# Optimization experiments

Hardware: AMD Instinct MI355X
Metric: run time of the kernel (lower is better)

The kernel has to match this reference:

```python
import jax, jax.numpy as jnp
import numpy as np

NUM_GROUPS = 32
NUM_HEADS = 8
EPS = 1e-5


def setup_inputs() -> dict:
    key = jax.random.key(0)
    ks = jax.random.split(key, 4)
    b, c, h, w = 16, 512, 32, 32
    x = jax.random.normal(ks[0], (b, c, h, w), dtype=jnp.float32)
    norm_w = jnp.ones((c,), dtype=jnp.float32)
    norm_b = jnp.zeros((c,), dtype=jnp.float32)
    qkv_w = jax.random.normal(ks[1], (3 * c, c), dtype=jnp.float32) * (1.0 / np.sqrt(c))
    qkv_b = jnp.zeros((3 * c,), dtype=jnp.float32)
    proj_w = jax.random.normal(ks[2], (c, c), dtype=jnp.float32) * (1.0 / np.sqrt(c))
    proj_b = jnp.zeros((c,), dtype=jnp.float32)
    return {"x": x, "norm_w": norm_w, "norm_b": norm_b,
            "qkv_w": qkv_w, "qkv_b": qkv_b, "proj_w": proj_w, "proj_b": proj_b}


def group_norm(x, weight, bias):
    b, c, h, w = x.shape
    xg = x.reshape(b, NUM_GROUPS, c // NUM_GROUPS, h * w)
    mean = xg.mean(axis=(2, 3), keepdims=True)
    var = xg.var(axis=(2, 3), keepdims=True)
    xn = (xg - mean) * jax.lax.rsqrt(var + EPS)
    xn = xn.reshape(b, c, h, w)
    return xn * weight[None, :, None, None] + bias[None, :, None, None]


def reference(x, norm_w, norm_b, qkv_w, qkv_b, proj_w, proj_b):
    b, c, h, w = x.shape
    n = h * w
    head = NUM_HEADS
    ch = c // head

    x_norm = group_norm(x, norm_w, norm_b)
    # 1x1 conv == channel matmul: [b,3c,n]
    xf = x_norm.reshape(b, c, n)
    qkv = jnp.einsum('oc,bcn->bon', qkv_w, xf) + qkv_b[None, :, None]
    q, k, v = jnp.split(qkv, 3, axis=1)  # each [b,c,n]
    q = q.reshape(b, head, ch, n) * (ch ** -0.5)
    k = k.reshape(b, head, ch, n)
    v = v.reshape(b, head, ch, n)

    attn = jnp.einsum('bhcn,bhcm->bhnm', q, k)
    attn = jax.nn.softmax(attn, axis=-1)
    out = jnp.einsum('bhnm,bhcm->bhcn', attn, v)  # [b,head,ch,n]
    out = out.reshape(b, c, n)
    out = jnp.einsum('oc,bcn->bon', proj_w, out) + proj_b[None, :, None]
    return x + out.reshape(b, c, h, w)
```

## Files before the change

### kernel.cpp

```cpp
#include <hip/hip_runtime.h>

typedef short short8 __attribute__((ext_vector_type(8)));
typedef short short4v __attribute__((ext_vector_type(4)));
typedef float f32x4 __attribute__((ext_vector_type(4)));

#define B_   16
#define C_   512
#define N_   1024
#define NH_  8
#define CH_  64
#define G_   32
#define CPG_ 16

__device__ inline float b2f(unsigned int u) {
    union { unsigned int i; float f; } v; v.i = u << 16; return v.f;
}
__device__ inline unsigned short f2b(float f) {
    union { float f; unsigned int i; } v; v.f = f;
    unsigned int r = v.i + 0x7fffu + ((v.i >> 16) & 1u);
    return (unsigned short)(r >> 16);
}
__device__ inline unsigned int pack2(float a, float b) {
    return (unsigned int)f2b(a) | ((unsigned int)f2b(b) << 16);
}
__device__ inline unsigned int asu(float f) {
    union { float f; unsigned int i; } v; v.f = f; return v.i;
}
__device__ inline unsigned int packtr(float a, float b) {
    return __builtin_amdgcn_perm(asu(b), asu(a), 0x07060302u);
}
__device__ inline void gload16(const void* g, void* l) {
    __builtin_amdgcn_global_load_lds(
        (const __attribute__((address_space(1))) void*)g,
        (__attribute__((address_space(3))) void*)l, 16, 0, 0);
}

__global__ __launch_bounds__(256) void gnconv_kernel(const float* __restrict__ x,
                                                     const float* __restrict__ nw,
                                                     const float* __restrict__ nb,
                                                     unsigned short* __restrict__ xnT,
                                                     const float* __restrict__ qkvw,
                                                     const float* __restrict__ projw,
                                                     unsigned short* __restrict__ wq,
                                                     unsigned short* __restrict__ wp)
{
    __shared__ float red[8];
    int t = threadIdx.x;

    if (blockIdx.x >= 512) {
        const int NQ = 3 * C_ * C_;
        int idx = (((int)blockIdx.x - 512) * 256 + t) * 8;
        const float* src; unsigned short* dst; int j;
        if (idx < NQ) { src = qkvw;  dst = wq; j = idx; }
        else          { src = projw; dst = wp; j = idx - NQ; }
        float4 u0 = *(const float4*)(src + j);
        float4 u1 = *(const float4*)(src + j + 4);
        uint4 p;
        p.x = pack2(u0.x, u0.y); p.y = pack2(u0.z, u0.w);
        p.z = pack2(u1.x, u1.y); p.w = pack2(u1.z, u1.w);
        *(uint4*)(dst + j) = p;
        return;
    }

    int b = blockIdx.x >> 5, g = blockIdx.x & 31;
    const float* base = x + ((size_t)(b * C_ + g * CPG_)) * N_;

    float s = 0.f, ss = 0.f;
    for (int it = 0; it < 16; ++it) {
        int idx = (it * 256 + t) * 4;
        float4 u = *(const float4*)(base + idx);
        s  += u.x + u.y + u.z + u.w;
        ss += u.x * u.x + u.y * u.y + u.z * u.z + u.w * u.w;
    }
#pragma unroll
    for (int off = 1; off < 64; off <<= 1) {
        s  += __shfl_xor(s, off);
        ss += __shfl_xor(ss, off);
    }
    int wv = t >> 6;
    if ((t & 63) == 0) { red[wv * 2] = s; red[wv * 2 + 1] = ss; }
    __syncthreads();
    s  = red[0] + red[2] + red[4] + red[6];
    ss = red[1] + red[3] + red[5] + red[7];
    float mean = s * (1.f / 16384.f);
    float var  = ss * (1.f / 16384.f) - mean * mean;
    float rstd = rsqrtf(var + 1e-5f);

    float sc[16], sh[16];
#pragma unroll
    for (int ch = 0; ch < 16; ++ch) {
        float wv_ = nw[g * CPG_ + ch];
        float bv_ = nb[g * CPG_ + ch];
        sc[ch] = wv_ * rstd;
        sh[ch] = bv_ - mean * sc[ch];
    }

#pragma unroll
    for (int nbi = 0; nbi < 2; ++nbi) {
        int n = nbi * 512 + t * 2;
        float2 v[16];
#pragma unroll
        for (int ch = 0; ch < 16; ++ch)
            v[ch] = *(const float2*)(base + (size_t)ch * N_ + n);
#pragma unroll
        for (int col = 0; col < 2; ++col) {
            float f[16];
#pragma unroll
            for (int ch = 0; ch < 16; ++ch) {
                float xv = col ? v[ch].y : v[ch].x;
                f[ch] = xv * sc[ch] + sh[ch];
            }
            uint4 o0, o1;
            o0.x = pack2(f[0], f[1]);  o0.y = pack2(f[2], f[3]);
            o0.z = pack2(f[4], f[5]);  o0.w = pack2(f[6], f[7]);
            o1.x = pack2(f[8], f[9]);  o1.y = pack2(f[10], f[11]);
            o1.z = pack2(f[12], f[13]); o1.w = pack2(f[14], f[15]);
            unsigned short* dst = xnT + ((size_t)(b * N_ + n + col)) * C_ + g * CPG_;
            *(uint4*)dst = o0;
            *(uint4*)(dst + 8) = o1;
        }
    }
}

__global__ __launch_bounds__(256) void qkv_kernel(const unsigned short* __restrict__ w,
                                                  const float* __restrict__ bias,
                                                  const unsigned short* __restrict__ xnT,
                                                  unsigned short* __restrict__ qT,
                                                  unsigned short* __restrict__ kT,
                                                  unsigned short* __restrict__ vv)
{
    __shared__ unsigned short Als[128 * 64], Bls[128 * 64];
    int t = threadIdx.x;
    int n0 = blockIdx.x * 128, m0 = blockIdx.y * 128, b = blockIdx.z;
    int lane = t & 63, wv = t >> 6;
    int l = lane & 15, qd = lane >> 4;
    int wm = (wv >> 1) * 64, wn = (wv & 1) * 64;
    f32x4 acc[4][4] = {};
    const unsigned short* Bbase = xnT + ((size_t)(b * N_ + n0)) * C_;

    int grow = lane >> 3, gcol = ((lane & 7) ^ grow) * 8;
    const unsigned short* pA[4]; const unsigned short* pB[4];
    unsigned short* lA[4]; unsigned short* lB[4];
#pragma unroll
    for (int g = 0; g < 4; ++g) {
        int r = wv * 32 + g * 8 + grow;
        pA[g] = w + (size_t)(m0 + r) * C_ + gcol;
        pB[g] = Bbase + (size_t)r * C_ + gcol;
        lA[g] = &Als[(wv * 32 + g * 8) * 64];
        lB[g] = &Bls[(wv * 32 + g * 8) * 64];
    }

    for (int kk = 0; kk < 8; ++kk) {
        int ko = kk * 64;
#pragma unroll
        for (int g = 0; g < 4; ++g) {
            gload16(pA[g] + ko, lA[g]);
            gload16(pB[g] + ko, lB[g]);
        }
        __builtin_amdgcn_s_waitcnt(0);
        __syncthreads();
#pragma unroll
        for (int ks = 0; ks < 2; ++ks) {
            short8 aF[4], bF[4];
#pragma unroll
            for (int i = 0; i < 4; ++i) {
                int ra = wm + i * 16 + l;
                aF[i] = *(const short8*)&Als[ra * 64 + (((ks * 4 + qd) ^ (l & 7)) * 8)];
                int rb = wn + i * 16 + l;
                bF[i] = *(const short8*)&Bls[rb * 64 + (((ks * 4 + qd) ^ (l & 7)) * 8)];
            }
#pragma unroll
            for (int mt = 0; mt < 4; ++mt)
#pragma unroll
                for (int nt = 0; nt < 4; ++nt)
                    acc[mt][nt] = __builtin_amdgcn_mfma_f32_16x16x32_bf16(aF[mt], bF[nt], acc[mt][nt], 0, 0, 0);
        }
        __syncthreads();
    }

    int o_base = m0 + wm;
    int sec = o_base >> 9;
    int oc = o_base & 511;
    int h = oc >> 6;
    float bv[4][4];
#pragma unroll
    for (int mt = 0; mt < 4; ++mt)
#pragma unroll
        for (int r = 0; r < 4; ++r)
            bv[mt][r] = bias[o_base + mt * 16 + qd * 4 + r];

    if (sec < 2) {
        unsigned short* dst = (sec == 0) ? qT : kT;
        float scl = (sec == 0) ? (0.125f * 1.44269504f) : 1.0f;
#pragma unroll
        for (int mt = 0; mt < 4; ++mt)
#pragma unroll
            for (int nt = 0; nt < 4; ++nt) {
                int n = n0 + wn + nt * 16 + l;
                ushort4 o;
                o.x = f2b((acc[mt][nt][0] + bv[mt][0]) * scl);
                o.y = f2b((acc[mt][nt][1] + bv[mt][1]) * scl);
                o.z = f2b((acc[mt][nt][2] + bv[mt][2]) * scl);
                o.w = f2b((acc[mt][nt][3] + bv[mt][3]) * scl);
                *(ushort4*)(dst + ((size_t)(b * NH_ + h) * N_ + n) * CH_ + mt * 16 + qd * 4) = o;
            }
    } else {
#pragma unroll
        for (int mt = 0; mt < 4; ++mt)
#pragma unroll
            for (int nt = 0; nt < 4; ++nt) {
                int n = n0 + wn + nt * 16 + l;
#pragma unroll
                for (int r = 0; r < 4; ++r) {
                    int ch = mt * 16 + qd * 4 + r;
                    vv[((size_t)(b * NH_ + h) * CH_ + ch) * N_ + n] = f2b(acc[mt][nt][r] + bv[mt][r]);
                }
            }
    }
}

__global__ __launch_bounds__(256, 4) void attn_kernel(const unsigned short* __restrict__ qT,
                                                      const unsigned short* __restrict__ kT,
                                                      const unsigned short* __restrict__ vv,
                                                      unsigned short* __restrict__ at)
{
    __shared__ unsigned short Ks[2][4096];
    __shared__ unsigned short Vs[2][4224];

    int t = threadIdx.x, lane = t & 63, wv = t >> 6;
    int l = lane & 15, qd = lane >> 4;
    int blk = blockIdx.x;
    int ibk = blk >> 7;
    int bh  = blk & 127;
    int h = bh & 7, b = bh >> 3;
    int i0 = ibk * 128 + wv * 32;
    const size_t hoff = (size_t)bh * (size_t)N_ * CH_;
    const unsigned short* qbase = qT + hoff;
    const unsigned short* kbase = kT + hoff;
    const unsigned short* vbase = vv + hoff;

    short8 qF[2][2];
#pragma unroll
    for (int it = 0; it < 2; ++it)
#pragma unroll
        for (int ks = 0; ks < 2; ++ks)
            qF[it][ks] = *(const short8*)(qbase + (size_t)(i0 + it * 16 + l) * CH_ + ks * 32 + qd * 8);

    int srow = t >> 2, p = t & 3;
    int sw = srow & 7, bb = p * 2;
    int d0 = srow * 64 + ((bb ^ sw) * 8);
    int d1 = srow * 64 + (((bb + 1) ^ sw) * 8);
    int lch = srow & 15, chtS = srow >> 4;
    int vblk = p * 4 + chtS;
    int vd[4];
#pragma unroll
    for (int w = 0; w < 4; ++w)
        vd[w] = vblk * 264 + (w * 16 + lch) * 4;
    const unsigned short* kSrc = kbase + (size_t)srow * CH_ + p * 16;
    const unsigned short* vSrc = vbase + (size_t)srow * N_ + p * 16;

    f32x4 Oa[4][2] = {};
    float lsum[2] = {0.f, 0.f};
    int swl = l & 7;

    uint4 ku0, ku1, vu0, vu1;
    {
        const uint4* kp = (const uint4*)(kSrc);
        ku0 = kp[0]; ku1 = kp[1];
        const uint4* vp2 = (const uint4*)(vSrc);
        vu0 = vp2[0]; vu1 = vp2[1];
        *(uint4*)&Ks[0][d0] = ku0; *(uint4*)&Ks[0][d1] = ku1;
        *(uint2*)&Vs[0][vd[0]] = make_uint2(vu0.x, vu0.y);
        *(uint2*)&Vs[0][vd[1]] = make_uint2(vu0.z, vu0.w);
        *(uint2*)&Vs[0][vd[2]] = make_uint2(vu1.x, vu1.y);
        *(uint2*)&Vs[0][vd[3]] = make_uint2(vu1.z, vu1.w);
        kp  = (const uint4*)(kSrc + 4096);
        ku0 = kp[0]; ku1 = kp[1];
        vp2 = (const uint4*)(vSrc + 64);
        vu0 = vp2[0]; vu1 = vp2[1];
    }

    for (int tile = 0; tile < 16; ++tile) {
        __syncthreads();
        if (tile < 15) {
            unsigned short* Kw = Ks[(tile + 1) & 1];
            unsigned short* Vw = Vs[(tile + 1) & 1];
            *(uint4*)&Kw[d0] = ku0; *(uint4*)&Kw[d1] = ku1;
            *(uint2*)&Vw[vd[0]] = make_uint2(vu0.x, vu0.y);
            *(uint2*)&Vw[vd[1]] = make_uint2(vu0.z, vu0.w);
            *(uint2*)&Vw[vd[2]] = make_uint2(vu1.x, vu1.y);
            *(uint2*)&Vw[vd[3]] = make_uint2(vu1.z, vu1.w);
            if (tile < 14) {
                const uint4* kp = (const uint4*)(kSrc + (size_t)(tile + 2) * 4096);
                ku0 = kp[0]; ku1 = kp[1];
                const uint4* vp2 = (const uint4*)(vSrc + (size_t)(tile + 2) * 64);
                vu0 = vp2[0]; vu1 = vp2[1];
            }
        }
        const unsigned short* Kb = Ks[tile & 1];
        const unsigned short* Vb = Vs[tile & 1];
#pragma unroll
        for (int jb = 0; jb < 2; ++jb) {
            short8 kA[2][2];
#pragma unroll
            for (int jt = 0; jt < 2; ++jt)
#pragma unroll
                for (int ks = 0; ks < 2; ++ks)
                    kA[jt][ks] = *(const short8*)&Kb[(jb * 32 + jt * 16 + l) * 64 + (((ks * 4 + qd) ^ swl) * 8)];
            f32x4 Sa[2][2] = {};
#pragma unroll
            for (int jt = 0; jt < 2; ++jt)
#pragma unroll
                for (int it = 0; it < 2; ++it)
#pragma unroll
                    for (int ks = 0; ks < 2; ++ks)
                        Sa[jt][it] = __builtin_amdgcn_mfma_f32_16x16x32_bf16(kA[jt][ks], qF[it][ks], Sa[jt][it], 0, 0, 0);
            unsigned int pk[2][2][2];
#pragma unroll
            for (int jt = 0; jt < 2; ++jt)
#pragma unroll
                for (int it = 0; it < 2; ++it) {
                    float p0 = __builtin_amdgcn_exp2f(Sa[jt][it][0]);
                    float p1 = __builtin_amdgcn_exp2f(Sa[jt][it][1]);
                    float p2 = __builtin_amdgcn_exp2f(Sa[jt][it][2]);
                    float p3 = __builtin_amdgcn_exp2f(Sa[jt][it][3]);
                    lsum[it] += (p0 + p1) + (p2 + p3);
                    pk[jt][it][0] = packtr(p0, p1);
                    pk[jt][it][1] = packtr(p2, p3);
                }
#pragma unroll
            for (int jt = 0; jt < 2; ++jt) {
                short4v vA[4];
#pragma unroll
                for (int cht = 0; cht < 4; ++cht) {
                    union { uint2 u; short4v s; } vr;
                    vr.u = *(const uint2*)&Vb[((jb * 2 + jt) * 4 + cht) * 264 + (qd * 16 + l) * 4];
                    vA[cht] = vr.s;
                }
#pragma unroll
                for (int it = 0; it < 2; ++it) {
                    union { unsigned int u[2]; short4v s; } ap;
                    ap.u[0] = pk[jt][it][0]; ap.u[1] = pk[jt][it][1];
#pragma unroll
                    for (int cht = 0; cht < 4; ++cht)
                        Oa[cht][it] = __builtin_amdgcn_mfma_f32_16x16x16bf16_1k(vA[cht], ap.s, Oa[cht][it], 0, 0, 0);
                }
            }
        }
    }

#pragma unroll
    for (int it = 0; it < 2; ++it) {
        float lt = lsum[it];
        lt += __shfl_xor(lt, 16);
        lt += __shfl_xor(lt, 32);
        float inv = 1.0f / lt;
        int i = i0 + it * 16 + l;
        unsigned short* dst = at + ((size_t)(b * N_ + i)) * C_ + h * CH_;
#pragma unroll
        for (int cht = 0; cht < 4; ++cht) {
            ushort4 o;
            o.x = f2b(Oa[cht][it][0] * inv);
            o.y = f2b(Oa[cht][it][1] * inv);
            o.z = f2b(Oa[cht][it][2] * inv);
            o.w = f2b(Oa[cht][it][3] * inv);
            *(ushort4*)(dst + cht * 16 + qd * 4) = o;
        }
    }
}

__global__ __launch_bounds__(256) void proj_kernel(const unsigned short* __restrict__ w,
                                                   const float* __restrict__ bias,
                                                   const unsigned short* __restrict__ at,
                                                   const float* __restrict__ x,
                                                   float* __restrict__ out)
{
    __shared__ unsigned short Als[128 * 64], Bls[128 * 64];
    int t = threadIdx.x;
    int n0 = blockIdx.x * 128, m0 = blockIdx.y * 128, b = blockIdx.z;
    int lane = t & 63, wv = t >> 6;
    int l = lane & 15, qd = lane >> 4;
    int wm = (wv >> 1) * 64, wn = (wv & 1) * 64;
    f32x4 acc[4][4] = {};
    const unsigned short* Bbase = at + ((size_t)(b * N_ + n0)) * C_;

    int grow = lane >> 3, gcol = ((lane & 7) ^ grow) * 8;
    const unsigned short* pA[4]; const unsigned short* pB[4];
    unsigned short* lA[4]; unsigned short* lB[4];
#pragma unroll
    for (int g = 0; g < 4; ++g) {
        int r = wv * 32 + g * 8 + grow;
        pA[g] = w + (size_t)(m0 + r) * C_ + gcol;
        pB[g] = Bbase + (size_t)r * C_ + gcol;
        lA[g] = &Als[(wv * 32 + g * 8) * 64];
        lB[g] = &Bls[(wv * 32 + g * 8) * 64];
    }

    for (int kk = 0; kk < 8; ++kk) {
        int ko = kk * 64;
#pragma unroll
        for (int g = 0; g < 4; ++g) {
            gload16(pA[g] + ko, lA[g]);
            gload16(pB[g] + ko, lB[g]);
        }
        __builtin_amdgcn_s_waitcnt(0);
        __syncthreads();
#pragma unroll
        for (int ks = 0; ks < 2; ++ks) {
            short8 aF[4], bF[4];
#pragma unroll
            for (int i = 0; i < 4; ++i) {
                int ra = wm + i * 16 + l;
                aF[i] = *(const short8*)&Als[ra * 64 + (((ks * 4 + qd) ^ (l & 7)) * 8)];
                int rb = wn + i * 16 + l;
                bF[i] = *(const short8*)&Bls[rb * 64 + (((ks * 4 + qd) ^ (l & 7)) * 8)];
            }
#pragma unroll
            for (int mt = 0; mt < 4; ++mt)
#pragma unroll
                for (int nt = 0; nt < 4; ++nt)
                    acc[mt][nt] = __builtin_amdgcn_mfma_f32_16x16x32_bf16(aF[mt], bF[nt], acc[mt][nt], 0, 0, 0);
        }
        __syncthreads();
    }

    float bv[4][4];
#pragma unroll
    for (int mt = 0; mt < 4; ++mt)
#pragma unroll
        for (int r = 0; r < 4; ++r)
            bv[mt][r] = bias[m0 + wm + mt * 16 + qd * 4 + r];

#pragma unroll
    for (int mt = 0; mt < 4; ++mt)
#pragma unroll
        for (int nt = 0; nt < 4; ++nt) {
            int n = n0 + wn + nt * 16 + l;
#pragma unroll
            for (int r = 0; r < 4; ++r) {
                int o = m0 + wm + mt * 16 + qd * 4 + r;
                size_t idx = ((size_t)b * C_ + o) * N_ + n;
                out[idx] = acc[mt][nt][r] + bv[mt][r] + x[idx];
            }
        }
}

extern "C" void kernel_launch(void* const* d_in, const int* in_sizes, int n_in,
                              void* d_out, int out_size, void* d_ws, size_t ws_size,
                              hipStream_t stream) {
    const float* x     = (const float*)d_in[0];
    const float* nw    = (const float*)d_in[1];
    const float* nb    = (const float*)d_in[2];
    const float* qkvw  = (const float*)d_in[3];
    const float* qkvb  = (const float*)d_in[4];
    const float* projw = (const float*)d_in[5];
    const float* projb = (const float*)d_in[6];
    float* out = (float*)d_out;
    char* ws = (char*)d_ws;
    const size_t SZ = (size_t)B_ * N_ * C_ * 2;
    unsigned short* xnT = (unsigned short*)(ws);
    unsigned short* qTp = (unsigned short*)(ws + SZ);
    unsigned short* kTp = (unsigned short*)(ws + 2 * SZ);
    unsigned short* vp  = (unsigned short*)(ws + 3 * SZ);
    unsigned short* atp = (unsigned short*)(ws);
    unsigned short* wq  = (unsigned short*)(ws + 4 * SZ);
    unsigned short* wp  = (unsigned short*)(ws + 4 * SZ + (size_t)3 * C_ * C_ * 2);

    hipLaunchKernelGGL(gnconv_kernel, dim3(1024), dim3(256), 0, stream, x, nw, nb, xnT, qkvw, projw, wq, wp);
    hipLaunchKernelGGL(qkv_kernel,    dim3(8, 12, B_), dim3(256), 0, stream, wq, qkvb, xnT, qTp, kTp, vp);
    hipLaunchKernelGGL(attn_kernel,   dim3(1024), dim3(256), 0, stream, qTp, kTp, vp, atp);
    hipLaunchKernelGGL(proj_kernel,   dim3(8, 4, B_), dim3(256), 0, stream, wp, projb, atp, x, out);
}
```

Before: 212.6 us.

## Double-buffer LDS in QKV and proj GEMMs and vectorize V stores via transposed MFMA

Both GEMM kernels switch from a single 64-wide K tile to two 32-wide LDS buffers. The next tile's global-to-LDS loads are issued before computing on the current one, so memory latency overlaps with MFMA work and one barrier per step goes away. In the QKV kernel, V-section blocks swap the MFMA operands to produce the transposed tile, which lets the V output be written as contiguous ushort4 stores instead of scattered 2-byte writes. This doubles the number of K iterations and changes the LDS swizzle, which adds loop overhead and risks new bank-conflict patterns.

Measured after the change: 232.8 us. 9.5% more time.

```diff
diff --git a/kernel.cpp b/kernel.cpp
--- a/kernel.cpp
+++ b/kernel.cpp
@@ -129,7 +129,7 @@
                                                   unsigned short* __restrict__ kT,
                                                   unsigned short* __restrict__ vv)
 {
-    __shared__ unsigned short Als[128 * 64], Bls[128 * 64];
+    __shared__ unsigned short Als[2][128 * 32], Bls[2][128 * 32];
     int t = threadIdx.x;
     int n0 = blockIdx.x * 128, m0 = blockIdx.y * 128, b = blockIdx.z;
     int lane = t & 63, wv = t >> 6;
@@ -137,59 +137,66 @@
     int wm = (wv >> 1) * 64, wn = (wv & 1) * 64;
     f32x4 acc[4][4] = {};
     const unsigned short* Bbase = xnT + ((size_t)(b * N_ + n0)) * C_;
-
-    int grow = lane >> 3, gcol = ((lane & 7) ^ grow) * 8;
-    const unsigned short* pA[4]; const unsigned short* pB[4];
-    unsigned short* lA[4]; unsigned short* lB[4];
-#pragma unroll
-    for (int g = 0; g < 4; ++g) {
-        int r = wv * 32 + g * 8 + grow;
-        pA[g] = w + (size_t)(m0 + r) * C_ + gcol;
-        pB[g] = Bbase + (size_t)r * C_ + gcol;
-        lA[g] = &Als[(wv * 32 + g * 8) * 64];
-        lB[g] = &Bls[(wv * 32 + g * 8) * 64];
-    }
-
-    for (int kk = 0; kk < 8; ++kk) {
-        int ko = kk * 64;
-#pragma unroll
-        for (int g = 0; g < 4; ++g) {
-            gload16(pA[g] + ko, lA[g]);
-            gload16(pB[g] + ko, lB[g]);
+    int isv = (m0 >= 1024);
+
+    int lr = lane >> 2, bpos = lane & 3;
+    int r0 = wv * 32 + lr, r1 = r0 + 16;
+    int c0 = (bpos ^ ((r0 >> 1) & 3)) * 8;
+    int c1 = (bpos ^ ((r1 >> 1) & 3)) * 8;
+    const unsigned short* gA0 = w + (size_t)(m0 + r0) * C_ + c0;
+    const unsigned short* gA1 = w + (size_t)(m0 + r1) * C_ + c1;
+    const unsigned short* gB0 = Bbase + (size_t)r0 * C_ + c0;
+    const unsigned short* gB1 = Bbase + (size_t)r1 * C_ + c1;
+    int lo0 = (wv * 32) * 32, lo1 = (wv * 32 + 16) * 32;
+    int aswz = (qd ^ ((l >> 1) & 3)) * 8;
+
+    gload16(gA0, &Als[0][lo0]); gload16(gA1, &Als[0][lo1]);
+    gload16(gB0, &Bls[0][lo0]); gload16(gB1, &Bls[0][lo1]);
+    __builtin_amdgcn_s_waitcnt(0);
+    __syncthreads();
+
+    for (int kk = 0; kk < 16; ++kk) {
+        if (kk < 15) {
+            int ko = (kk + 1) * 32;
+            int nb = (kk + 1) & 1;
+            gload16(gA0 + ko, &Als[nb][lo0]); gload16(gA1 + ko, &Als[nb][lo1]);
+            gload16(gB0 + ko, &Bls[nb][lo0]); gload16(gB1 + ko, &Bls[nb][lo1]);
+        }
+        const unsigned short* Ab = Als[kk & 1];
+        const unsigned short* Bb = Bls[kk & 1];
+        short8 aF[4], bF[4];
+#pragma unroll
+        for (int i = 0; i < 4; ++i) {
+            aF[i] = *(const short8*)&Ab[(wm + i * 16 + l) * 32 + aswz];
+            bF[i] = *(const short8*)&Bb[(wn + i * 16 + l) * 32 + aswz];
+        }
+        if (!isv) {
+#pragma unroll
+            for (int mt = 0; mt < 4; ++mt)
+#pragma unroll
+                for (int nt = 0; nt < 4; ++nt)
+                    acc[mt][nt] = __builtin_amdgcn_mfma_f32_16x16x32_bf16(aF[mt], bF[nt], acc[mt][nt], 0, 0, 0);
+        } else {
+#pragma unroll
+            for (int mt = 0; mt < 4; ++mt)
+#pragma unroll
+                for (int nt = 0; nt < 4; ++nt)
+                    acc[mt][nt] = __builtin_amdgcn_mfma_f32_16x16x32_bf16(bF[nt], aF[mt], acc[mt][nt], 0, 0, 0);
         }
         __builtin_amdgcn_s_waitcnt(0);
         __syncthreads();
-#pragma unroll
-        for (int ks = 0; ks < 2; ++ks) {
-            short8 aF[4], bF[4];
-#pragma unroll
-            for (int i = 0; i < 4; ++i) {
-                int ra = wm + i * 16 + l;
-                aF[i] = *(const short8*)&Als[ra * 64 + (((ks * 4 + qd) ^ (l & 7)) * 8)];
-                int rb = wn + i * 16 + l;
-                bF[i] = *(const short8*)&Bls[rb * 64 + (((ks * 4 + qd) ^ (l & 7)) * 8)];
-            }
-#pragma unroll
-            for (int mt = 0; mt < 4; ++mt)
-#pragma unroll
-                for (int nt = 0; nt < 4; ++nt)
-                    acc[mt][nt] = __builtin_amdgcn_mfma_f32_16x16x32_bf16(aF[mt], bF[nt], acc[mt][nt], 0, 0, 0);
-        }
-        __syncthreads();
-    }
-
-    int o_base = m0 + wm;
-    int sec = o_base >> 9;
-    int oc = o_base & 511;
-    int h = oc >> 6;
-    float bv[4][4];
-#pragma unroll
-    for (int mt = 0; mt < 4; ++mt)
-#pragma unroll
-        for (int r = 0; r < 4; ++r)
-            bv[mt][r] = bias[o_base + mt * 16 + qd * 4 + r];
-
-    if (sec < 2) {
+    }
+
+    if (!isv) {
+        int o_base = m0 + wm;
+        int sec = o_base >> 9;
+        int h = (o_base & 511) >> 6;
+        float bv[4][4];
+#pragma unroll
+        for (int mt = 0; mt < 4; ++mt)
+#pragma unroll
+            for (int r = 0; r < 4; ++r)
+                bv[mt][r] = bias[o_base + mt * 16 + qd * 4 + r];
         unsigned short* dst = (sec == 0) ? qT : kT;
         float scl = (sec == 0) ? (0.125f * 1.44269504f) : 1.0f;
 #pragma unroll
@@ -206,16 +213,23 @@
             }
     } else {
 #pragma unroll
-        for (int mt = 0; mt < 4; ++mt)
+        for (int mt = 0; mt < 4; ++mt) {
+            int och = m0 - 1024 + wm + mt * 16;
+            int h = och >> 6;
+            int chl = (och & 63) + l;
+            float bvl = bias[m0 + wm + mt * 16 + l];
+            unsigned short* vdst = vv + ((size_t)(b * NH_ + h) * CH_ + chl) * N_;
 #pragma unroll
             for (int nt = 0; nt < 4; ++nt) {
-                int n = n0 + wn + nt * 16 + l;
-#pragma unroll
-                for (int r = 0; r < 4; ++r) {
-                    int ch = mt * 16 + qd * 4 + r;
-                    vv[((size_t)(b * NH_ + h) * CH_ + ch) * N_ + n] = f2b(acc[mt][nt][r] + bv[mt][r]);
-                }
-            }
+                int n = n0 + wn + nt * 16 + qd * 4;
+                ushort4 o;
+                o.x = f2b(acc[mt][nt][0] + bvl);
+                o.y = f2b(acc[mt][nt][1] + bvl);
+                o.z = f2b(acc[mt][nt][2] + bvl);
+                o.w = f2b(acc[mt][nt][3] + bvl);
+                *(ushort4*)(vdst + n) = o;
+            }
+        }
     }
 }
 
@@ -375,7 +389,7 @@
                                                    const float* __restrict__ x,
                                                    float* __restrict__ out)
 {
-    __shared__ unsigned short Als[128 * 64], Bls[128 * 64];
+    __shared__ unsigned short Als[2][128 * 32], Bls[2][128 * 32];
     int t = threadIdx.x;
     int n0 = blockIdx.x * 128, m0 = blockIdx.y * 128, b = blockIdx.z;
     int lane = t & 63, wv = t >> 6;
@@ -384,43 +398,43 @@
     f32x4 acc[4][4] = {};
     const unsigned short* Bbase = at + ((size_t)(b * N_ + n0)) * C_;
 
-    int grow = lane >> 3, gcol = ((lane & 7) ^ grow) * 8;
-    const unsigned short* pA[4]; const unsigned short* pB[4];
-    unsigned short* lA[4]; unsigned short* lB[4];
-#pragma unroll
-    for (int g = 0; g < 4; ++g) {
-        int r = wv * 32 + g * 8 + grow;
-        pA[g] = w + (size_t)(m0 + r) * C_ + gcol;
-        pB[g] = Bbase + (size_t)r * C_ + gcol;
-        lA[g] = &Als[(wv * 32 + g * 8) * 64];
-        lB[g] = &Bls[(wv * 32 + g * 8) * 64];
-    }
-
-    for (int kk = 0; kk < 8; ++kk) {
-        int ko = kk * 64;
-#pragma unroll
-        for (int g = 0; g < 4; ++g) {
-            gload16(pA[g] + ko, lA[g]);
-            gload16(pB[g] + ko, lB[g]);
-        }
+    int lr = lane >> 2, bpos = lane & 3;
+    int r0 = wv * 32 + lr, r1 = r0 + 16;
+    int c0 = (bpos ^ ((r0 >> 1) & 3)) * 8;
+    int c1 = (bpos ^ ((r1 >> 1) & 3)) * 8;
+    const unsigned short* gA0 = w + (size_t)(m0 + r0) * C_ + c0;
+    const unsigned short* gA1 = w + (size_t)(m0 + r1) * C_ + c1;
+    const unsigned short* gB0 = Bbase + (size_t)r0 * C_ + c0;
+    const unsigned short* gB1 = Bbase + (size_t)r1 * C_ + c1;
+    int lo0 = (wv * 32) * 32, lo1 = (wv * 32 + 16) * 32;
+    int aswz = (qd ^ ((l >> 1) & 3)) * 8;
+
+    gload16(gA0, &Als[0][lo0]); gload16(gA1, &Als[0][lo1]);
+    gload16(gB0, &Bls[0][lo0]); gload16(gB1, &Bls[0][lo1]);
+    __builtin_amdgcn_s_waitcnt(0);
+    __syncthreads();
+
+    for (int kk = 0; kk < 16; ++kk) {
+        if (kk < 15) {
+            int ko = (kk + 1) * 32;
+            int nb = (kk + 1) & 1;
+            gload16(gA0 + ko, &Als[nb][lo0]); gload16(gA1 + ko, &Als[nb][lo1]);
+            gload16(gB0 + ko, &Bls[nb][lo0]); gload16(gB1 + ko, &Bls[nb][lo1]);
+        }
+        const unsigned short* Ab = Als[kk & 1];
+        const unsigned short* Bb = Bls[kk & 1];
+        short8 aF[4], bF[4];
+#pragma unroll
+        for (int i = 0; i < 4; ++i) {
+            aF[i] = *(const short8*)&Ab[(wm + i * 16 + l) * 32 + aswz];
+            bF[i] = *(const short8*)&Bb[(wn + i * 16 + l) * 32 + aswz];
+        }
+#pragma unroll
+        for (int mt = 0; mt < 4; ++mt)
+#pragma unroll
+            for (int nt = 0; nt < 4; ++nt)
+                acc[mt][nt] = __builtin_amdgcn_mfma_f32_16x16x32_bf16(aF[mt], bF[nt], acc[mt][nt], 0, 0, 0);
         __builtin_amdgcn_s_waitcnt(0);
-        __syncthreads();
-#pragma unroll
-        for (int ks = 0; ks < 2; ++ks) {
-            short8 aF[4], bF[4];
-#pragma unroll
-            for (int i = 0; i < 4; ++i) {
-                int ra = wm + i * 16 + l;
-                aF[i] = *(const short8*)&Als[ra * 64 + (((ks * 4 + qd) ^ (l & 7)) * 8)];
-                int rb = wn + i * 16 + l;
-                bF[i] = *(const short8*)&Bls[rb * 64 + (((ks * 4 + qd) ^ (l & 7)) * 8)];
-            }
-#pragma unroll
-            for (int mt = 0; mt < 4; ++mt)
-#pragma unroll
-                for (int nt = 0; nt < 4; ++nt)
-                    acc[mt][nt] = __builtin_amdgcn_mfma_f32_16x16x32_bf16(aF[mt], bF[nt], acc[mt][nt], 0, 0, 0);
-        }
         __syncthreads();
     }
 
```
